# Performance work log

Hardware: AMD Instinct MI355X
Metric: run time of the kernel (lower is better)

Reference implementation:

```python
import jax, jax.numpy as jnp
import numpy as np

D_MODEL = 512
N_HEADS = 8
D_FF = 2048
B, L = 4, 2048
EPS = 1e-5


def _layernorm(x, g, b):
    mu = jnp.mean(x, axis=-1, keepdims=True)
    var = jnp.mean(jnp.square(x - mu), axis=-1, keepdims=True)
    return (x - mu) * jax.lax.rsqrt(var + EPS) * g + b


def setup_inputs() -> dict:
    key = jax.random.key(0)
    ks = jax.random.split(key, 8)
    s = 0.02
    return {
        'x': jax.random.normal(ks[0], (B, L, D_MODEL), jnp.float32),
        'Wq': jax.random.normal(ks[1], (D_MODEL, D_MODEL), jnp.float32) * s,
        'bq': jnp.zeros((D_MODEL,), jnp.float32),
        'Wk': jax.random.normal(ks[2], (D_MODEL, D_MODEL), jnp.float32) * s,
        'bk': jnp.zeros((D_MODEL,), jnp.float32),
        'Wv': jax.random.normal(ks[3], (D_MODEL, D_MODEL), jnp.float32) * s,
        'bv': jnp.zeros((D_MODEL,), jnp.float32),
        'Wo': jax.random.normal(ks[4], (D_MODEL, D_MODEL), jnp.float32) * s,
        'bo': jnp.zeros((D_MODEL,), jnp.float32),
        'W1': jax.random.normal(ks[5], (D_MODEL, D_FF), jnp.float32) * s,
        'b1': jnp.zeros((D_FF,), jnp.float32),
        'W2': jax.random.normal(ks[6], (D_FF, D_MODEL), jnp.float32) * s,
        'b2': jnp.zeros((D_MODEL,), jnp.float32),
        'g1': jnp.ones((D_MODEL,), jnp.float32),
        'be1': jnp.zeros((D_MODEL,), jnp.float32),
        'g2': jnp.ones((D_MODEL,), jnp.float32),
        'be2': jnp.zeros((D_MODEL,), jnp.float32),
    }


def reference(x, Wq, bq, Wk, bk, Wv, bv, Wo, bo, W1, b1, W2, b2, g1, be1, g2, be2):
    B_, L_, D = x.shape
    H = N_HEADS
    E = D // H
    q = (x @ Wq + bq).reshape(B_, L_, H, E)
    k = (x @ Wk + bk).reshape(B_, L_, H, E)
    v = (x @ Wv + bv).reshape(B_, L_, H, E)
    scale = 1.0 / jnp.sqrt(jnp.float32(E))
    # full [B,H,L,S] scores (mask_flag=False -> no causal mask)
    scores = jnp.einsum('blhe,bshe->bhls', q, k)
    A = jax.nn.softmax(scale * scores, axis=-1)
    V = jnp.einsum('bhls,bshd->blhd', A, v).reshape(B_, L_, D)
    attn_out = V @ Wo + bo
    x = _layernorm(x + attn_out, g1, be1)
    h = jax.nn.gelu(x @ W1 + b1, approximate=False)  # torch nn.GELU default = exact erf
    x = _layernorm(x + (h @ W2 + b2), g2, be2)
    return x
```

## Files before the change

kernel.cpp:

```cpp
#include <hip/hip_runtime.h>
#include <math.h>

#define DM 512
#define LSEQ 2048
#define BATCH 4
#define NH 8
#define EH 64
#define DFF 2048
#define MTOK (BATCH*LSEQ)
#define QKVW 1536
#define QSCL 0.18033688011112042f

using short8  = __attribute__((ext_vector_type(8))) short;
using floatx4 = __attribute__((ext_vector_type(4))) float;

__device__ __forceinline__ short f2b(float f) {
    unsigned u = __float_as_uint(f);
    return (short)((u + 0x7FFFu + ((u >> 16) & 1u)) >> 16);
}
__device__ __forceinline__ float b2f(short s) {
    return __uint_as_float(((unsigned)(unsigned short)s) << 16);
}
__device__ __forceinline__ void load_lds16(const short* g, short* l) {
    __builtin_amdgcn_global_load_lds(
        (const __attribute__((address_space(1))) void*)g,
        (__attribute__((address_space(3))) void*)l, 16, 0, 0);
}

__global__ __launch_bounds__(256) void transpose_cvt(
    const float* __restrict__ in, short* __restrict__ out, int R, int C)
{
    __shared__ float t[64][65];
    const int tid = threadIdx.x;
    const int r0 = blockIdx.y * 64, c0 = blockIdx.x * 64;
    const int r = tid >> 2, cs = (tid & 3) * 16;
    const float* ip = in + (long)(r0 + r) * C + c0 + cs;
    #pragma unroll
    for (int i = 0; i < 4; ++i) {
        float4 v = *(const float4*)(ip + i * 4);
        t[r][cs + i*4 + 0] = v.x; t[r][cs + i*4 + 1] = v.y;
        t[r][cs + i*4 + 2] = v.z; t[r][cs + i*4 + 3] = v.w;
    }
    __syncthreads();
    short tmp[16];
    #pragma unroll
    for (int j = 0; j < 16; ++j) tmp[j] = f2b(t[cs + j][r]);
    short* op = out + (long)(c0 + r) * R + r0 + cs;
    *(float4*)op       = *(float4*)&tmp[0];
    *(float4*)(op + 8) = *(float4*)&tmp[8];
}

__global__ void fuse_bias_kernel(const float* __restrict__ bq,
                                 const float* __restrict__ bk,
                                 const float* __restrict__ bv,
                                 float* __restrict__ bqkv)
{
    int i = blockIdx.x * 256 + threadIdx.x;
    if (i < QKVW)
        bqkv[i] = (i < 512) ? bq[i] : (i < 1024 ? bk[i - 512] : bv[i - 1024]);
}

__global__ __launch_bounds__(256) void cvt_f32_bf16(
    const float* __restrict__ in, short* __restrict__ out)
{
    const int i = (blockIdx.x * 256 + threadIdx.x) * 8;
    float4 a = *(const float4*)(in + i);
    float4 b = *(const float4*)(in + i + 4);
    short t[8] = { f2b(a.x), f2b(a.y), f2b(a.z), f2b(a.w),
                   f2b(b.x), f2b(b.y), f2b(b.z), f2b(b.w) };
    *(float4*)(out + i) = *(float4*)t;
}

template<int DO_GELU, int QKV>
__global__ __launch_bounds__(256) void mfma_gemm(
    const short* __restrict__ A, const short* __restrict__ Bt,
    const float* __restrict__ bias, short* __restrict__ C,
    short* __restrict__ VtOut, int M, int N, int K, int lda, int ldc)
{
    __shared__ short As[128][32];
    __shared__ short Bs[128][32];

    const int tid  = threadIdx.x;
    const int wave = tid >> 6;
    const int lane = tid & 63;
    const int qd   = lane >> 4;
    const int sl   = lane & 15;
    const int m0 = blockIdx.y * 128;
    const int n0 = blockIdx.x * 128;
    const int wm = (wave & 1) * 64;
    const int wn = (wave >> 1) * 64;
    const int srow = lane >> 2;
    const int scol = (lane & 3) * 8;

    floatx4 acc[4][4];
    const floatx4 fz = {0.f, 0.f, 0.f, 0.f};
    #pragma unroll
    for (int i = 0; i < 4; ++i)
        #pragma unroll
        for (int j = 0; j < 4; ++j) acc[i][j] = fz;

    for (int k0 = 0; k0 < K; k0 += 32) {
        #pragma unroll
        for (int it = 0; it < 2; ++it) {
            const int rg = wave * 2 + it;
            const int row = rg * 16 + srow;
            load_lds16(A  + (long)(m0 + row) * lda + k0 + scol, &As[rg * 16][0]);
            load_lds16(Bt + (long)(n0 + row) * K   + k0 + scol, &Bs[rg * 16][0]);
        }
        __syncthreads();

        short8 af[4], bf[4];
        #pragma unroll
        for (int t = 0; t < 4; ++t) {
            af[t] = *(const short8*)&As[wm + t*16 + sl][qd * 8];
            bf[t] = *(const short8*)&Bs[wn + t*16 + sl][qd * 8];
        }
        #pragma unroll
        for (int i = 0; i < 4; ++i)
            #pragma unroll
            for (int j = 0; j < 4; ++j)
                acc[i][j] = __builtin_amdgcn_mfma_f32_16x16x32_bf16(
                    af[i], bf[j], acc[i][j], 0, 0, 0);
        __syncthreads();
    }

    #pragma unroll
    for (int j = 0; j < 4; ++j) {
        const int col = n0 + wn + j*16 + sl;
        const float bv = bias[col];
        #pragma unroll
        for (int i = 0; i < 4; ++i) {
            #pragma unroll
            for (int r = 0; r < 4; ++r) {
                const int row = m0 + wm + i*16 + qd*4 + r;
                float v = acc[i][j][r] + bv;
                if (DO_GELU) v = 0.5f * v * (1.0f + erff(v * 0.70710678118654752f));
                if (QKV) {
                    if (col < 512) v *= QSCL;
                    const short bb = f2b(v);
                    if (col < 1024) {
                        C[(long)row * 1024 + col] = bb;
                    } else {
                        const int e = col - 1024;
                        const int b_ = row >> 11, l = row & 2047;
                        VtOut[(((long)(b_*8 + (e >> 6))) * 64 + (e & 63)) * 2048 + l] = bb;
                    }
                } else {
                    C[(long)row * ldc + col] = f2b(v);
                }
            }
        }
    }
}

__global__ __launch_bounds__(256) void mfma_attn(
    const short* __restrict__ QK, const short* __restrict__ VtG,
    short* __restrict__ O)
{
    __shared__ short Qs[128][72];
    __shared__ short Ks[64][72];
    __shared__ short Vs[64][72];
    __shared__ short Ps[4][32][72];

    const int tid  = threadIdx.x;
    const int wave = tid >> 6;
    const int lane = tid & 63;
    const int qd   = lane >> 4;
    const int sl   = lane & 15;

    const int blk = blockIdx.x;
    const int qt = blk & 15;
    const int h  = (blk >> 4) & 7;
    const int b  = blk >> 7;
    const int tok0 = b * LSEQ;
    const int q0 = qt * 128;

    {
        const int lr = tid >> 1, lc = (tid & 1) * 32;
        const short* qp = QK + (long)(tok0 + q0 + lr) * 1024 + h * EH + lc;
        *(float4*)&Qs[lr][lc]      = *(const float4*)(qp);
        *(float4*)&Qs[lr][lc + 8]  = *(const float4*)(qp + 8);
        *(float4*)&Qs[lr][lc + 16] = *(const float4*)(qp + 16);
        *(float4*)&Qs[lr][lc + 24] = *(const float4*)(qp + 24);
    }
    __syncthreads();

    short8 aq[2][2];
    #pragma unroll
    for (int q2 = 0; q2 < 2; ++q2)
        #pragma unroll
        for (int ks = 0; ks < 2; ++ks)
            aq[q2][ks] = *(const short8*)&Qs[wave*32 + q2*16 + sl][ks*32 + qd*8];

    float l_i[2][4] = {};
    floatx4 oacc[2][4];
    const floatx4 fz = {0.f, 0.f, 0.f, 0.f};
    #pragma unroll
    for (int q2 = 0; q2 < 2; ++q2)
        #pragma unroll
        for (int t = 0; t < 4; ++t) oacc[q2][t] = fz;

    const int klr = tid >> 2, klc = (tid & 3) * 16;
    const long vbase = ((long)(b * NH + h)) * EH * 2048;

    for (int kt = 0; kt < LSEQ / 64; ++kt) {
        const int k0 = kt * 64;
        __syncthreads();
        {
            const short* kp = QK + (long)(tok0 + k0 + klr) * 1024 + 512 + h * EH + klc;
            *(float4*)&Ks[klr][klc]     = *(const float4*)kp;
            *(float4*)&Ks[klr][klc + 8] = *(const float4*)(kp + 8);
            const short* vp = VtG + vbase + (long)klr * 2048 + k0 + klc;
            *(float4*)&Vs[klr][klc]     = *(const float4*)vp;
            *(float4*)&Vs[klr][klc + 8] = *(const float4*)(vp + 8);
        }
        __syncthreads();

        floatx4 s[2][4];
        #pragma unroll
        for (int q2 = 0; q2 < 2; ++q2)
            #pragma unroll
            for (int t = 0; t < 4; ++t) s[q2][t] = fz;
        #pragma unroll
        for (int ks = 0; ks < 2; ++ks)
            #pragma unroll
            for (int t = 0; t < 4; ++t) {
                short8 bk = *(const short8*)&Ks[t*16 + sl][ks*32 + qd*8];
                s[0][t] = __builtin_amdgcn_mfma_f32_16x16x32_bf16(aq[0][ks], bk, s[0][t], 0, 0, 0);
                s[1][t] = __builtin_amdgcn_mfma_f32_16x16x32_bf16(aq[1][ks], bk, s[1][t], 0, 0, 0);
            }

        #pragma unroll
        for (int q2 = 0; q2 < 2; ++q2)
            #pragma unroll
            for (int t = 0; t < 4; ++t) {
                const int pg = (((t*2 + (sl >> 3)) ^ qd) << 3) | (sl & 7);
                #pragma unroll
                for (int r = 0; r < 4; ++r) {
                    const float pv = __builtin_amdgcn_exp2f(s[q2][t][r]);
                    l_i[q2][r] += pv;
                    Ps[wave][q2*16 + qd*4 + r][pg] = (short)(__float_as_uint(pv) >> 16);
                }
            }

        #pragma unroll
        for (int ks = 0; ks < 2; ++ks) {
            const int pgr = ((ks*4 + qd) ^ ((sl >> 2) & 3)) * 8;
            short8 ap0 = *(const short8*)&Ps[wave][sl][pgr];
            short8 ap1 = *(const short8*)&Ps[wave][16 + sl][pgr];
            #pragma unroll
            for (int t = 0; t < 4; ++t) {
                short8 bv = *(const short8*)&Vs[t*16 + sl][ks*32 + qd*8];
                oacc[0][t] = __builtin_amdgcn_mfma_f32_16x16x32_bf16(ap0, bv, oacc[0][t], 0, 0, 0);
                oacc[1][t] = __builtin_amdgcn_mfma_f32_16x16x32_bf16(ap1, bv, oacc[1][t], 0, 0, 0);
            }
        }
    }

    float linv[2][4];
    #pragma unroll
    for (int q2 = 0; q2 < 2; ++q2)
        #pragma unroll
        for (int r = 0; r < 4; ++r) {
            float l = l_i[q2][r];
            l += __shfl_xor(l, 1);
            l += __shfl_xor(l, 2);
            l += __shfl_xor(l, 4);
            l += __shfl_xor(l, 8);
            linv[q2][r] = 1.0f / l;
        }
    #pragma unroll
    for (int q2 = 0; q2 < 2; ++q2)
        #pragma unroll
        for (int t = 0; t < 4; ++t)
            #pragma unroll
            for (int r = 0; r < 4; ++r) {
                const int row = tok0 + q0 + wave*32 + q2*16 + qd*4 + r;
                const int col = h * EH + t*16 + sl;
                O[(long)row * DM + col] = f2b(oacc[q2][t][r] * linv[q2][r]);
            }
}

template<int X_BF16, int OUT_F32>
__global__ __launch_bounds__(256) void add_ln_kernel(
    const void* __restrict__ Xv, const short* __restrict__ R,
    const float* __restrict__ g, const float* __restrict__ beta,
    void* __restrict__ outv)
{
    const int row = blockIdx.x;
    const int tid = threadIdx.x;
    float x0, x1;
    if (X_BF16) {
        const short* xp = (const short*)Xv + (long)row * DM;
        x0 = b2f(xp[tid]); x1 = b2f(xp[tid + 256]);
    } else {
        const float* xp = (const float*)Xv + (long)row * DM;
        x0 = xp[tid]; x1 = xp[tid + 256];
    }
    const short* rp = R + (long)row * DM;
    const float v0 = x0 + b2f(rp[tid]);
    const float v1 = x1 + b2f(rp[tid + 256]);
    float s = v0 + v1, sq = v0*v0 + v1*v1;
    #pragma unroll
    for (int o = 32; o > 0; o >>= 1) {
        s  += __shfl_down(s, o);
        sq += __shfl_down(sq, o);
    }
    __shared__ float ss[4], ssq[4];
    const int wid = tid >> 6, lane = tid & 63;
    if (lane == 0) { ss[wid] = s; ssq[wid] = sq; }
    __syncthreads();
    const float S  = ss[0] + ss[1] + ss[2] + ss[3];
    const float SQ = ssq[0] + ssq[1] + ssq[2] + ssq[3];
    const float mean = S * (1.0f / DM);
    const float var  = SQ * (1.0f / DM) - mean * mean;
    const float rstd = rsqrtf(var + 1e-5f);
    const float o0 = (v0 - mean) * rstd * g[tid] + beta[tid];
    const float o1 = (v1 - mean) * rstd * g[tid + 256] + beta[tid + 256];
    if (OUT_F32) {
        float* op = (float*)outv + (long)row * DM;
        op[tid] = o0; op[tid + 256] = o1;
    } else {
        short* op = (short*)outv + (long)row * DM;
        op[tid] = f2b(o0); op[tid + 256] = f2b(o1);
    }
}

extern "C" void kernel_launch(void* const* d_in, const int* in_sizes, int n_in,
                              void* d_out, int out_size, void* d_ws, size_t ws_size,
                              hipStream_t stream)
{
    const float* x   = (const float*)d_in[0];
    const float* Wq  = (const float*)d_in[1];
    const float* bq  = (const float*)d_in[2];
    const float* Wk  = (const float*)d_in[3];
    const float* bk  = (const float*)d_in[4];
    const float* Wv  = (const float*)d_in[5];
    const float* bv  = (const float*)d_in[6];
    const float* Wo  = (const float*)d_in[7];
    const float* bo  = (const float*)d_in[8];
    const float* W1  = (const float*)d_in[9];
    const float* b1  = (const float*)d_in[10];
    const float* W2  = (const float*)d_in[11];
    const float* b2  = (const float*)d_in[12];
    const float* g1  = (const float*)d_in[13];
    const float* be1 = (const float*)d_in[14];
    const float* g2  = (const float*)d_in[15];
    const float* be2 = (const float*)d_in[16];
    float* out = (float*)d_out;

    short* ws    = (short*)d_ws;
    short* Wqkvt = ws;
    short* Wot   = Wqkvt + 786432;
    short* W1t   = Wot + 262144;
    short* W2t   = W1t + 1048576;
    float* bqkv  = (float*)(W2t + 1048576);
    short* xb    = (short*)(bqkv + 1536);
    short* qk    = xb + 4194304;
    short* VtG   = qk + 8388608;
    short* Ob    = VtG + 4194304;
    short* res   = Ob + 4194304;
    short* hbuf  = qk;

    const dim3 blk(256);

    fuse_bias_kernel<<<dim3(6), blk, 0, stream>>>(bq, bk, bv, bqkv);
    transpose_cvt<<<dim3(8, 8),  blk, 0, stream>>>(Wq, Wqkvt,              DM, DM);
    transpose_cvt<<<dim3(8, 8),  blk, 0, stream>>>(Wk, Wqkvt + 512L * DM,  DM, DM);
    transpose_cvt<<<dim3(8, 8),  blk, 0, stream>>>(Wv, Wqkvt + 1024L * DM, DM, DM);
    transpose_cvt<<<dim3(8, 8),  blk, 0, stream>>>(Wo, Wot, DM, DM);
    transpose_cvt<<<dim3(32, 8), blk, 0, stream>>>(W1, W1t, DM, DFF);
    transpose_cvt<<<dim3(8, 32), blk, 0, stream>>>(W2, W2t, DFF, DM);
    cvt_f32_bf16<<<dim3(2048), blk, 0, stream>>>(x, xb);

    mfma_gemm<0, 1><<<dim3(12, 64), blk, 0, stream>>>(
        xb, Wqkvt, bqkv, qk, VtG, MTOK, QKVW, DM, DM, 0);

    mfma_attn<<<dim3(512), blk, 0, stream>>>(qk, VtG, Ob);

    mfma_gemm<0, 0><<<dim3(4, 64), blk, 0, stream>>>(
        Ob, Wot, bo, res, nullptr, MTOK, DM, DM, DM, DM);

    add_ln_kernel<0, 0><<<dim3(MTOK), blk, 0, stream>>>(x, res, g1, be1, xb);

    mfma_gemm<1, 0><<<dim3(16, 64), blk, 0, stream>>>(
        xb, W1t, b1, hbuf, nullptr, MTOK, DFF, DM, DM, DFF);

    mfma_gemm<0, 0><<<dim3(4, 64), blk, 0, stream>>>(
        hbuf, W2t, b2, res, nullptr, MTOK, DM, DFF, DFF, DM);

    add_ln_kernel<1, 1><<<dim3(MTOK), blk, 0, stream>>>(xb, res, g2, be2, out);
}
```

Measured before the change: 331.7 us.

## Merge prep kernels, halve N-tile for narrow GEMMs, register-prefetch K/V in attention

Result: slower. 373.8 us (+12.7%).

```diff
diff --git a/kernel.cpp b/kernel.cpp
--- a/kernel.cpp
+++ b/kernel.cpp
@@ -27,14 +27,57 @@
         (__attribute__((address_space(3))) void*)l, 16, 0, 0);
 }
 
-__global__ __launch_bounds__(256) void transpose_cvt(
-    const float* __restrict__ in, short* __restrict__ out, int R, int C)
+__global__ __launch_bounds__(256) void prep_kernel(
+    const float* __restrict__ Wq, const float* __restrict__ Wk,
+    const float* __restrict__ Wv, const float* __restrict__ Wo,
+    const float* __restrict__ W1, const float* __restrict__ W2,
+    const float* __restrict__ x,
+    const float* __restrict__ bq, const float* __restrict__ bk,
+    const float* __restrict__ bv,
+    short* __restrict__ Wqkvt, short* __restrict__ Wot,
+    short* __restrict__ W1t, short* __restrict__ W2t,
+    short* __restrict__ xb, float* __restrict__ bqkv)
 {
     __shared__ float t[64][65];
+    const int bid = blockIdx.x;
     const int tid = threadIdx.x;
-    const int r0 = blockIdx.y * 64, c0 = blockIdx.x * 64;
+
+    if (bid >= 2880) {
+        #pragma unroll
+        for (int j = 0; j < 6; ++j) {
+            const int i = j * 256 + tid;
+            bqkv[i] = (i < 512) ? bq[i] : (i < 1024 ? bk[i - 512] : bv[i - 1024]);
+        }
+        return;
+    }
+    if (bid >= 832) {
+        const long i = ((long)(bid - 832) * 256 + tid) * 8;
+        float4 a = *(const float4*)(x + i);
+        float4 b = *(const float4*)(x + i + 4);
+        short tt[8] = { f2b(a.x), f2b(a.y), f2b(a.z), f2b(a.w),
+                        f2b(b.x), f2b(b.y), f2b(b.z), f2b(b.w) };
+        *(float4*)(xb + i) = *(float4*)tt;
+        return;
+    }
+    const float* src; short* dst; int C, R, bx, by;
+    if (bid < 256) {
+        const int w = bid >> 6, sub = bid & 63;
+        src = (w == 0) ? Wq : (w == 1) ? Wk : Wv;
+        dst = Wqkvt + (long)w * 262144;
+        R = 512; C = 512; bx = sub & 7; by = sub >> 3;
+    } else if (bid < 320) {
+        const int sub = bid - 256;
+        src = Wo; dst = Wot; R = 512; C = 512; bx = sub & 7; by = sub >> 3;
+    } else if (bid < 576) {
+        const int sub = bid - 320;
+        src = W1; dst = W1t; R = 512; C = 2048; bx = sub & 31; by = sub >> 5;
+    } else {
+        const int sub = bid - 576;
+        src = W2; dst = W2t; R = 2048; C = 512; bx = sub & 7; by = sub >> 3;
+    }
+    const int r0 = by * 64, c0 = bx * 64;
     const int r = tid >> 2, cs = (tid & 3) * 16;
-    const float* ip = in + (long)(r0 + r) * C + c0 + cs;
+    const float* ip = src + (long)(r0 + r) * C + c0 + cs;
     #pragma unroll
     for (int i = 0; i < 4; ++i) {
         float4 v = *(const float4*)(ip + i * 4);
@@ -45,40 +88,21 @@
     short tmp[16];
     #pragma unroll
     for (int j = 0; j < 16; ++j) tmp[j] = f2b(t[cs + j][r]);
-    short* op = out + (long)(c0 + r) * R + r0 + cs;
+    short* op = dst + (long)(c0 + r) * R + r0 + cs;
     *(float4*)op       = *(float4*)&tmp[0];
     *(float4*)(op + 8) = *(float4*)&tmp[8];
 }
 
-__global__ void fuse_bias_kernel(const float* __restrict__ bq,
-                                 const float* __restrict__ bk,
-                                 const float* __restrict__ bv,
-                                 float* __restrict__ bqkv)
-{
-    int i = blockIdx.x * 256 + threadIdx.x;
-    if (i < QKVW)
-        bqkv[i] = (i < 512) ? bq[i] : (i < 1024 ? bk[i - 512] : bv[i - 1024]);
-}
-
-__global__ __launch_bounds__(256) void cvt_f32_bf16(
-    const float* __restrict__ in, short* __restrict__ out)
-{
-    const int i = (blockIdx.x * 256 + threadIdx.x) * 8;
-    float4 a = *(const float4*)(in + i);
-    float4 b = *(const float4*)(in + i + 4);
-    short t[8] = { f2b(a.x), f2b(a.y), f2b(a.z), f2b(a.w),
-                   f2b(b.x), f2b(b.y), f2b(b.z), f2b(b.w) };
-    *(float4*)(out + i) = *(float4*)t;
-}
-
-template<int DO_GELU, int QKV>
+template<int TN, int DO_GELU, int QKV>
 __global__ __launch_bounds__(256) void mfma_gemm(
     const short* __restrict__ A, const short* __restrict__ Bt,
     const float* __restrict__ bias, short* __restrict__ C,
     short* __restrict__ VtOut, int M, int N, int K, int lda, int ldc)
 {
+    constexpr int NJ = TN / 32;
+    constexpr int NB = TN / 64;
     __shared__ short As[128][32];
-    __shared__ short Bs[128][32];
+    __shared__ short Bs[TN][32];
 
     const int tid  = threadIdx.x;
     const int wave = tid >> 6;
@@ -86,46 +110,50 @@
     const int qd   = lane >> 4;
     const int sl   = lane & 15;
     const int m0 = blockIdx.y * 128;
-    const int n0 = blockIdx.x * 128;
+    const int n0 = blockIdx.x * TN;
     const int wm = (wave & 1) * 64;
-    const int wn = (wave >> 1) * 64;
+    const int wn = (wave >> 1) * (TN / 2);
     const int srow = lane >> 2;
     const int scol = (lane & 3) * 8;
 
-    floatx4 acc[4][4];
+    floatx4 acc[4][NJ];
     const floatx4 fz = {0.f, 0.f, 0.f, 0.f};
     #pragma unroll
     for (int i = 0; i < 4; ++i)
         #pragma unroll
-        for (int j = 0; j < 4; ++j) acc[i][j] = fz;
+        for (int j = 0; j < NJ; ++j) acc[i][j] = fz;
 
     for (int k0 = 0; k0 < K; k0 += 32) {
         #pragma unroll
         for (int it = 0; it < 2; ++it) {
             const int rg = wave * 2 + it;
-            const int row = rg * 16 + srow;
-            load_lds16(A  + (long)(m0 + row) * lda + k0 + scol, &As[rg * 16][0]);
-            load_lds16(Bt + (long)(n0 + row) * K   + k0 + scol, &Bs[rg * 16][0]);
+            load_lds16(A + (long)(m0 + rg*16 + srow) * lda + k0 + scol, &As[rg * 16][0]);
+        }
+        #pragma unroll
+        for (int it = 0; it < NB; ++it) {
+            const int rg = wave * NB + it;
+            load_lds16(Bt + (long)(n0 + rg*16 + srow) * K + k0 + scol, &Bs[rg * 16][0]);
         }
         __syncthreads();
 
-        short8 af[4], bf[4];
-        #pragma unroll
-        for (int t = 0; t < 4; ++t) {
+        short8 af[4], bf[NJ];
+        #pragma unroll
+        for (int t = 0; t < 4; ++t)
             af[t] = *(const short8*)&As[wm + t*16 + sl][qd * 8];
+        #pragma unroll
+        for (int t = 0; t < NJ; ++t)
             bf[t] = *(const short8*)&Bs[wn + t*16 + sl][qd * 8];
-        }
         #pragma unroll
         for (int i = 0; i < 4; ++i)
             #pragma unroll
-            for (int j = 0; j < 4; ++j)
+            for (int j = 0; j < NJ; ++j)
                 acc[i][j] = __builtin_amdgcn_mfma_f32_16x16x32_bf16(
                     af[i], bf[j], acc[i][j], 0, 0, 0);
         __syncthreads();
     }
 
     #pragma unroll
-    for (int j = 0; j < 4; ++j) {
+    for (int j = 0; j < NJ; ++j) {
         const int col = n0 + wn + j*16 + sl;
         const float bv = bias[col];
         #pragma unroll
@@ -153,13 +181,66 @@
     }
 }
 
-__global__ __launch_bounds__(256) void mfma_attn(
+#define ATTN_MFMA(a, b, c) __builtin_amdgcn_mfma_f32_16x16x32_bf16(a, b, c, 0, 0, 0)
+
+#define LOAD_BK(KT, DST) { \
+    const short* kp_ = QK + kbase + (long)(KT) * 64 * 1024; \
+    _Pragma("unroll") \
+    for (int t_ = 0; t_ < 4; ++t_) \
+        _Pragma("unroll") \
+        for (int ks_ = 0; ks_ < 2; ++ks_) \
+            DST[t_*2 + ks_] = *(const short8*)(kp_ + (long)(t_*16 + sl) * 1024 + ks_*32 + qd*8); }
+
+#define ATTN_BODY(KT, BKC, BKN) { \
+    __builtin_amdgcn_s_barrier(); \
+    short8 bvv[8]; \
+    const short* vp_ = VtG + vbase + (KT) * 64; \
+    _Pragma("unroll") \
+    for (int t_ = 0; t_ < 4; ++t_) \
+        _Pragma("unroll") \
+        for (int ks_ = 0; ks_ < 2; ++ks_) \
+            bvv[t_*2 + ks_] = *(const short8*)(vp_ + (long)(t_*16 + sl) * 2048 + ks_*32 + qd*8); \
+    LOAD_BK(((KT) + 1) & 31, BKN); \
+    floatx4 s[2][4]; \
+    _Pragma("unroll") \
+    for (int q2 = 0; q2 < 2; ++q2) \
+        _Pragma("unroll") \
+        for (int t_ = 0; t_ < 4; ++t_) s[q2][t_] = fz; \
+    _Pragma("unroll") \
+    for (int ks_ = 0; ks_ < 2; ++ks_) \
+        _Pragma("unroll") \
+        for (int t_ = 0; t_ < 4; ++t_) { \
+            s[0][t_] = ATTN_MFMA(aq[0][ks_], BKC[t_*2 + ks_], s[0][t_]); \
+            s[1][t_] = ATTN_MFMA(aq[1][ks_], BKC[t_*2 + ks_], s[1][t_]); \
+        } \
+    _Pragma("unroll") \
+    for (int q2 = 0; q2 < 2; ++q2) \
+        _Pragma("unroll") \
+        for (int t_ = 0; t_ < 4; ++t_) { \
+            const int pg = (((t_*2 + (sl >> 3)) ^ qd) << 3) | (sl & 7); \
+            _Pragma("unroll") \
+            for (int r = 0; r < 4; ++r) { \
+                const float pv = __builtin_amdgcn_exp2f(s[q2][t_][r]); \
+                l_i[q2][r] += pv; \
+                Ps[wave][q2*16 + qd*4 + r][pg] = (short)(__float_as_uint(pv) >> 16); \
+            } \
+        } \
+    _Pragma("unroll") \
+    for (int ks_ = 0; ks_ < 2; ++ks_) { \
+        const int pgr = ((ks_*4 + qd) ^ ((sl >> 2) & 3)) * 8; \
+        short8 ap0 = *(const short8*)&Ps[wave][sl][pgr]; \
+        short8 ap1 = *(const short8*)&Ps[wave][16 + sl][pgr]; \
+        _Pragma("unroll") \
+        for (int t_ = 0; t_ < 4; ++t_) { \
+            oacc[0][t_] = ATTN_MFMA(ap0, bvv[t_*2 + ks_], oacc[0][t_]); \
+            oacc[1][t_] = ATTN_MFMA(ap1, bvv[t_*2 + ks_], oacc[1][t_]); \
+        } \
+    } }
+
+__global__ __launch_bounds__(256, 2) void mfma_attn(
     const short* __restrict__ QK, const short* __restrict__ VtG,
     short* __restrict__ O)
 {
-    __shared__ short Qs[128][72];
-    __shared__ short Ks[64][72];
-    __shared__ short Vs[64][72];
     __shared__ short Ps[4][32][72];
 
     const int tid  = threadIdx.x;
@@ -168,29 +249,31 @@
     const int qd   = lane >> 4;
     const int sl   = lane & 15;
 
-    const int blk = blockIdx.x;
-    const int qt = blk & 15;
-    const int h  = (blk >> 4) & 7;
-    const int b  = blk >> 7;
+    const int bid = blockIdx.x;
+    const int h  = bid & 7;
+    const int b  = (bid >> 3) & 3;
+    const int qt = bid >> 5;
     const int tok0 = b * LSEQ;
     const int q0 = qt * 128;
+    const long kbase = (long)tok0 * 1024 + 512 + h * EH;
+    const long vbase = ((long)(b * NH + h)) * EH * 2048;
 
     {
-        const int lr = tid >> 1, lc = (tid & 1) * 32;
+        const int lr = tid >> 1;
+        const int lc = (tid & 1) * 32;
         const short* qp = QK + (long)(tok0 + q0 + lr) * 1024 + h * EH + lc;
-        *(float4*)&Qs[lr][lc]      = *(const float4*)(qp);
-        *(float4*)&Qs[lr][lc + 8]  = *(const float4*)(qp + 8);
-        *(float4*)&Qs[lr][lc + 16] = *(const float4*)(qp + 16);
-        *(float4*)&Qs[lr][lc + 24] = *(const float4*)(qp + 24);
-    }
-    __syncthreads();
-
+        short* dp = &Ps[wave][lr & 31][lc];
+        *(float4*)(dp)      = *(const float4*)(qp);
+        *(float4*)(dp + 8)  = *(const float4*)(qp + 8);
+        *(float4*)(dp + 16) = *(const float4*)(qp + 16);
+        *(float4*)(dp + 24) = *(const float4*)(qp + 24);
+    }
     short8 aq[2][2];
     #pragma unroll
     for (int q2 = 0; q2 < 2; ++q2)
         #pragma unroll
         for (int ks = 0; ks < 2; ++ks)
-            aq[q2][ks] = *(const short8*)&Qs[wave*32 + q2*16 + sl][ks*32 + qd*8];
+            aq[q2][ks] = *(const short8*)&Ps[wave][q2*16 + sl][ks*32 + qd*8];
 
     float l_i[2][4] = {};
     floatx4 oacc[2][4];
@@ -200,61 +283,11 @@
         #pragma unroll
         for (int t = 0; t < 4; ++t) oacc[q2][t] = fz;
 
-    const int klr = tid >> 2, klc = (tid & 3) * 16;
-    const long vbase = ((long)(b * NH + h)) * EH * 2048;
-
-    for (int kt = 0; kt < LSEQ / 64; ++kt) {
-        const int k0 = kt * 64;
-        __syncthreads();
-        {
-            const short* kp = QK + (long)(tok0 + k0 + klr) * 1024 + 512 + h * EH + klc;
-            *(float4*)&Ks[klr][klc]     = *(const float4*)kp;
-            *(float4*)&Ks[klr][klc + 8] = *(const float4*)(kp + 8);
-            const short* vp = VtG + vbase + (long)klr * 2048 + k0 + klc;
-            *(float4*)&Vs[klr][klc]     = *(const float4*)vp;
-            *(float4*)&Vs[klr][klc + 8] = *(const float4*)(vp + 8);
-        }
-        __syncthreads();
-
-        floatx4 s[2][4];
-        #pragma unroll
-        for (int q2 = 0; q2 < 2; ++q2)
-            #pragma unroll
-            for (int t = 0; t < 4; ++t) s[q2][t] = fz;
-        #pragma unroll
-        for (int ks = 0; ks < 2; ++ks)
-            #pragma unroll
-            for (int t = 0; t < 4; ++t) {
-                short8 bk = *(const short8*)&Ks[t*16 + sl][ks*32 + qd*8];
-                s[0][t] = __builtin_amdgcn_mfma_f32_16x16x32_bf16(aq[0][ks], bk, s[0][t], 0, 0, 0);
-                s[1][t] = __builtin_amdgcn_mfma_f32_16x16x32_bf16(aq[1][ks], bk, s[1][t], 0, 0, 0);
-            }
-
-        #pragma unroll
-        for (int q2 = 0; q2 < 2; ++q2)
-            #pragma unroll
-            for (int t = 0; t < 4; ++t) {
-                const int pg = (((t*2 + (sl >> 3)) ^ qd) << 3) | (sl & 7);
-                #pragma unroll
-                for (int r = 0; r < 4; ++r) {
-                    const float pv = __builtin_amdgcn_exp2f(s[q2][t][r]);
-                    l_i[q2][r] += pv;
-                    Ps[wave][q2*16 + qd*4 + r][pg] = (short)(__float_as_uint(pv) >> 16);
-                }
-            }
-
-        #pragma unroll
-        for (int ks = 0; ks < 2; ++ks) {
-            const int pgr = ((ks*4 + qd) ^ ((sl >> 2) & 3)) * 8;
-            short8 ap0 = *(const short8*)&Ps[wave][sl][pgr];
-            short8 ap1 = *(const short8*)&Ps[wave][16 + sl][pgr];
-            #pragma unroll
-            for (int t = 0; t < 4; ++t) {
-                short8 bv = *(const short8*)&Vs[t*16 + sl][ks*32 + qd*8];
-                oacc[0][t] = __builtin_amdgcn_mfma_f32_16x16x32_bf16(ap0, bv, oacc[0][t], 0, 0, 0);
-                oacc[1][t] = __builtin_amdgcn_mfma_f32_16x16x32_bf16(ap1, bv, oacc[1][t], 0, 0, 0);
-            }
-        }
+    short8 bkA[8], bkB[8];
+    LOAD_BK(0, bkA);
+    for (int kt = 0; kt < 32; kt += 2) {
+        ATTN_BODY(kt,     bkA, bkB);
+        ATTN_BODY(kt + 1, bkB, bkA);
     }
 
     float linv[2][4];
@@ -364,29 +397,24 @@
 
     const dim3 blk(256);
 
-    fuse_bias_kernel<<<dim3(6), blk, 0, stream>>>(bq, bk, bv, bqkv);
-    transpose_cvt<<<dim3(8, 8),  blk, 0, stream>>>(Wq, Wqkvt,              DM, DM);
-    transpose_cvt<<<dim3(8, 8),  blk, 0, stream>>>(Wk, Wqkvt + 512L * DM,  DM, DM);
-    transpose_cvt<<<dim3(8, 8),  blk, 0, stream>>>(Wv, Wqkvt + 1024L * DM, DM, DM);
-    transpose_cvt<<<dim3(8, 8),  blk, 0, stream>>>(Wo, Wot, DM, DM);
-    transpose_cvt<<<dim3(32, 8), blk, 0, stream>>>(W1, W1t, DM, DFF);
-    transpose_cvt<<<dim3(8, 32), blk, 0, stream>>>(W2, W2t, DFF, DM);
-    cvt_f32_bf16<<<dim3(2048), blk, 0, stream>>>(x, xb);
-
-    mfma_gemm<0, 1><<<dim3(12, 64), blk, 0, stream>>>(
+    prep_kernel<<<dim3(2881), blk, 0, stream>>>(
+        Wq, Wk, Wv, Wo, W1, W2, x, bq, bk, bv,
+        Wqkvt, Wot, W1t, W2t, xb, bqkv);
+
+    mfma_gemm<128, 0, 1><<<dim3(12, 64), blk, 0, stream>>>(
         xb, Wqkvt, bqkv, qk, VtG, MTOK, QKVW, DM, DM, 0);
 
     mfma_attn<<<dim3(512), blk, 0, stream>>>(qk, VtG, Ob);
 
-    mfma_gemm<0, 0><<<dim3(4, 64), blk, 0, stream>>>(
+    mfma_gemm<64, 0, 0><<<dim3(8, 64), blk, 0, stream>>>(
         Ob, Wot, bo, res, nullptr, MTOK, DM, DM, DM, DM);
 
     add_ln_kernel<0, 0><<<dim3(MTOK), blk, 0, stream>>>(x, res, g1, be1, xb);
 
-    mfma_gemm<1, 0><<<dim3(16, 64), blk, 0, stream>>>(
+    mfma_gemm<128, 1, 0><<<dim3(16, 64), blk, 0, stream>>>(
         xb, W1t, b1, hbuf, nullptr, MTOK, DFF, DM, DM, DFF);
 
-    mfma_gemm<0, 0><<<dim3(4, 64), blk, 0, stream>>>(
+    mfma_gemm<64, 0, 0><<<dim3(8, 64), blk, 0, stream>>>(
         hbuf, W2t, b2, res, nullptr, MTOK, DM, DFF, DFF, DM);
 
     add_ln_kernel<1, 1><<<dim3(MTOK), blk, 0, stream>>>(xb, res, g2, be2, out);
```
